# Kernel tuning notes

Measured on AMD Instinct MI355X. Metric: run time of the kernel, lower is better.

The kernel has to match this reference:

```python
import jax, jax.numpy as jnp
import numpy as np

QMAX = 255.0  # 8-bit uniform affine quantization


def _round_ste(x):
    # straight-through estimator round (identity gradient)
    return x + jax.lax.stop_gradient(jnp.round(x) - x)


def _fake_quant(x, scale, zero_point):
    # uniform affine quantize-dequantize, as in DAQuant's UniformAffineQuantizer
    zp = _round_ste(zero_point)
    q = jnp.clip(_round_ste(x / scale) + zp, 0.0, QMAX)
    return (q - zp) * scale


def setup_inputs() -> dict:
    key = jax.random.key(0)
    k1, k2, k3, k4, k5 = jax.random.split(key, 5)
    B, S, H, I = 64, 197, 1024, 4096
    hidden_states = jax.random.normal(k1, (B, S, H), dtype=jnp.float32)
    weight = jax.random.normal(k2, (I, H), dtype=jnp.float32) * 0.02
    bias = jax.random.normal(k3, (I,), dtype=jnp.float32) * 0.02
    # per-output-channel weight quant params, per-tensor activation quant params
    w_scale = jax.random.uniform(k4, (I, 1), dtype=jnp.float32) * 1e-3 + 1e-4
    w_zero = jnp.full((I, 1), 128.0, dtype=jnp.float32)
    a_scale = jnp.float32(8.0 / QMAX)  # covers roughly [-4, 4] of activations
    a_zero = jnp.float32(128.0)
    return {
        "hidden_states": hidden_states,
        "weight": weight,
        "bias": bias,
        "w_scale": w_scale,
        "w_zero": w_zero,
        "a_scale": a_scale,
        "a_zero": a_zero,
    }


def reference(hidden_states, weight, bias, w_scale, w_zero, a_scale, a_zero):
    # fake-quant activation (per-tensor) and weight (per-output-channel)
    x_dq = _fake_quant(hidden_states, a_scale, a_zero)        # [B,S,H]
    w_dq = _fake_quant(weight, w_scale, w_zero)               # [I,H]
    y = jnp.einsum('bsh,ih->bsi', x_dq, w_dq) + bias          # [B,S,I]
    return jax.nn.gelu(y, approximate=False)                  # exact GELU (torch default)
```

## Files before the change

kernel.cpp:

```cpp
#include <hip/hip_runtime.h>
#include <hip/hip_bf16.h>

typedef __attribute__((ext_vector_type(4))) int i32x4;
typedef __attribute__((ext_vector_type(4))) float f32x4;

#define K_DIM 1024
#define I_DIM 4096
#define BK3 64
#define NT3 (K_DIM / BK3)

__device__ __forceinline__ float fakeq_int(float x, float s, float zp) {
    float q = fminf(fmaxf(rintf(x / s) + zp, 0.0f), 255.0f);
    return q - zp;
}

__device__ __forceinline__ float gelu_tanh(float y) {
    float y2 = y * y;
    float z = y * fmaf(0.0356774081f, y2, 0.7978845608f);
    return y / (1.0f + __expf(-2.0f * z));
}

__global__ void quant_x_kernel(const float* __restrict__ x, signed char* __restrict__ Aq,
                               const float* __restrict__ a_scale, const float* __restrict__ a_zero,
                               long long n) {
    long long i = ((long long)blockIdx.x * blockDim.x + threadIdx.x) * 8;
    if (i >= n) return;
    float s = a_scale[0];
    float zp = rintf(a_zero[0]);
    float4 v0 = *(const float4*)(x + i);
    float4 v1 = *(const float4*)(x + i + 4);
    int q0 = (int)fakeq_int(v0.x, s, zp), q1 = (int)fakeq_int(v0.y, s, zp);
    int q2 = (int)fakeq_int(v0.z, s, zp), q3 = (int)fakeq_int(v0.w, s, zp);
    int q4 = (int)fakeq_int(v1.x, s, zp), q5 = (int)fakeq_int(v1.y, s, zp);
    int q6 = (int)fakeq_int(v1.z, s, zp), q7 = (int)fakeq_int(v1.w, s, zp);
    int lo = (q0 & 255) | ((q1 & 255) << 8) | ((q2 & 255) << 16) | ((q3 & 255) << 24);
    int hi = (q4 & 255) | ((q5 & 255) << 8) | ((q6 & 255) << 16) | ((q7 & 255) << 24);
    *(int2*)(Aq + i) = make_int2(lo, hi);
}

__global__ void quant_w_kernel(const float* __restrict__ w, signed char* __restrict__ Wq,
                               const float* __restrict__ w_scale, const float* __restrict__ w_zero,
                               long long n) {
    long long i = ((long long)blockIdx.x * blockDim.x + threadIdx.x) * 8;
    if (i >= n) return;
    long long row = i >> 10;
    float s = w_scale[row];
    float zp = rintf(w_zero[row]);
    float4 v0 = *(const float4*)(w + i);
    float4 v1 = *(const float4*)(w + i + 4);
    int q0 = (int)fakeq_int(v0.x, s, zp), q1 = (int)fakeq_int(v0.y, s, zp);
    int q2 = (int)fakeq_int(v0.z, s, zp), q3 = (int)fakeq_int(v0.w, s, zp);
    int q4 = (int)fakeq_int(v1.x, s, zp), q5 = (int)fakeq_int(v1.y, s, zp);
    int q6 = (int)fakeq_int(v1.z, s, zp), q7 = (int)fakeq_int(v1.w, s, zp);
    int lo = (q0 & 255) | ((q1 & 255) << 8) | ((q2 & 255) << 16) | ((q3 & 255) << 24);
    int hi = (q4 & 255) | ((q5 & 255) << 8) | ((q6 & 255) << 16) | ((q7 & 255) << 24);
    *(int2*)(Wq + i) = make_int2(lo, hi);
}

#define GLL(SRC, DST)                                                         \
    __builtin_amdgcn_global_load_lds(                                         \
        (const __attribute__((address_space(1))) void*)(SRC),                 \
        (__attribute__((address_space(3))) void*)(DST), 16, 0, 0)

#define STAGE(TT, BUF)                                          \
    do {                                                        \
        GLL(pA0 + (TT) * BK3, As + (BUF) * 8192 + dA);          \
        GLL(pA1 + (TT) * BK3, As + (BUF) * 8192 + 4096 + dA);   \
        GLL(pB0 + (TT) * BK3, Bs + (BUF) * 8192 + dA);          \
        GLL(pB1 + (TT) * BK3, Bs + (BUF) * 8192 + 4096 + dA);   \
    } while (0)

__global__ __launch_bounds__(256, 3) void gemm_gelu_kernel(
    const signed char* __restrict__ Aq,
    const signed char* __restrict__ Wq,
    const float* __restrict__ bias,
    const float* __restrict__ w_scale,
    const float* __restrict__ a_scale,
    float* __restrict__ out,
    int M, int Ntiles) {
    __shared__ alignas(16) signed char As[3 * 128 * BK3];
    __shared__ alignas(16) signed char Bs[3 * 128 * BK3];

    int nwg = gridDim.x, bid = blockIdx.x;
    int xcd = bid & 7, lin = bid >> 3;
    int q8 = nwg >> 3, r8 = nwg & 7;
    int swz = (xcd < r8 ? xcd * (q8 + 1) : r8 * (q8 + 1) + (xcd - r8) * q8) + lin;
    int mt = swz / Ntiles, nt = swz % Ntiles;

    int tid = threadIdx.x;
    int wave = tid >> 6, lane = tid & 63;
    int wr = wave >> 1, wc = wave & 1;

    long long mrow0 = (long long)mt * 128;
    int ncol0 = nt * 128;

    int r0 = tid >> 2;
    int slotsrc = ((tid & 3) - ((tid >> 3) & 3)) & 3;
    long long mmax = (long long)M - 1;
    long long raA0 = mrow0 + r0;        if (raA0 > mmax) raA0 = mmax;
    long long raA1 = mrow0 + 64 + r0;   if (raA1 > mmax) raA1 = mmax;
    const signed char* pA0 = Aq + raA0 * K_DIM + slotsrc * 16;
    const signed char* pA1 = Aq + raA1 * K_DIM + slotsrc * 16;
    const signed char* pB0 = Wq + ((long long)ncol0 + r0) * K_DIM + slotsrc * 16;
    const signed char* pB1 = Wq + ((long long)ncol0 + 64 + r0) * K_DIM + slotsrc * 16;
    int dA = tid * 16;

    int koffb = (((lane >> 4) + ((lane >> 1) & 3)) & 3) * 16;
    int arowb = wr * 64 + (lane & 15);
    int browb = wc * 64 + (lane & 15);

    i32x4 acc[4][4];
#pragma unroll
    for (int m = 0; m < 4; ++m)
#pragma unroll
        for (int n = 0; n < 4; ++n) acc[m][n] = (i32x4)0;

    STAGE(0, 0);
    STAGE(1, 1);
    asm volatile("s_waitcnt vmcnt(4)" ::: "memory");
    __builtin_amdgcn_s_barrier();

    int buf = 0, bs2 = 2;
    for (int t = 0; t < NT3; ++t) {
        if (t + 2 < NT3) STAGE(t + 2, bs2);

        i32x4 a[4], b[4];
#pragma unroll
        for (int mi = 0; mi < 4; ++mi)
            a[mi] = *(const i32x4*)(As + buf * 8192 + (arowb + mi * 16) * BK3 + koffb);
#pragma unroll
        for (int n = 0; n < 4; ++n)
            b[n] = *(const i32x4*)(Bs + buf * 8192 + (browb + n * 16) * BK3 + koffb);

        __builtin_amdgcn_s_setprio(1);
#pragma unroll
        for (int mi = 0; mi < 4; ++mi)
#pragma unroll
            for (int n = 0; n < 4; ++n)
                acc[mi][n] = __builtin_amdgcn_mfma_i32_16x16x64_i8(a[mi], b[n], acc[mi][n], 0, 0, 0);
        __builtin_amdgcn_s_setprio(0);

        if (t + 2 < NT3) {
            asm volatile("s_waitcnt vmcnt(4)" ::: "memory");
        } else if (t + 1 < NT3) {
            asm volatile("s_waitcnt vmcnt(0)" ::: "memory");
        }
        if (t + 1 < NT3) __builtin_amdgcn_s_barrier();

        buf = (buf == 2) ? 0 : buf + 1;
        bs2 = (bs2 == 2) ? 0 : bs2 + 1;
    }

    float asc = a_scale[0];
    long long row0 = mrow0 + wr * 64;
    int colb = ncol0 + wc * 64 + (lane & 15);
    int rsubE = (lane >> 4) * 4;
    bool fullTile = (mrow0 + 128 <= (long long)M);
    if (fullTile) {
#pragma unroll
        for (int n = 0; n < 4; ++n) {
            int col = colb + n * 16;
            float sc = asc * w_scale[col];
            float bz = bias[col];
#pragma unroll
            for (int m = 0; m < 4; ++m) {
                long long rb = row0 + m * 16 + rsubE;
#pragma unroll
                for (int rg = 0; rg < 4; ++rg) {
                    float y = (float)acc[m][n][rg] * sc + bz;
                    out[(rb + rg) * I_DIM + col] = gelu_tanh(y);
                }
            }
        }
    } else {
#pragma unroll
        for (int n = 0; n < 4; ++n) {
            int col = colb + n * 16;
            float sc = asc * w_scale[col];
            float bz = bias[col];
#pragma unroll
            for (int m = 0; m < 4; ++m) {
                long long rb = row0 + m * 16 + rsubE;
#pragma unroll
                for (int rg = 0; rg < 4; ++rg) {
                    long long rowi = rb + rg;
                    if (rowi < M) {
                        float y = (float)acc[m][n][rg] * sc + bz;
                        out[rowi * I_DIM + col] = gelu_tanh(y);
                    }
                }
            }
        }
    }
}

__global__ void fallback_kernel(const float* __restrict__ x, const float* __restrict__ w,
                                const float* __restrict__ bias, const float* __restrict__ w_scale,
                                const float* __restrict__ w_zero, const float* __restrict__ a_scale,
                                const float* __restrict__ a_zero, float* __restrict__ out,
                                long long M) {
    long long gid = (long long)blockIdx.x * blockDim.x + threadIdx.x;
    if (gid >= M * I_DIM) return;
    int i = (int)(gid & (I_DIM - 1));
    long long row = gid >> 12;
    float as = a_scale[0], az = rintf(a_zero[0]);
    float wsc = w_scale[i], wz = rintf(w_zero[i]);
    const float* xr = x + row * K_DIM;
    const float* wrp = w + (long long)i * K_DIM;
    float accf = 0.0f;
    for (int k = 0; k < K_DIM; ++k)
        accf += fakeq_int(xr[k], as, az) * fakeq_int(wrp[k], wsc, wz);
    float y = accf * as * wsc + bias[i];
    out[gid] = 0.5f * y * (1.0f + erff(y * 0.70710678118654752f));
}

extern "C" void kernel_launch(void* const* d_in, const int* in_sizes, int n_in,
                              void* d_out, int out_size, void* d_ws, size_t ws_size,
                              hipStream_t stream) {
    const float* x       = (const float*)d_in[0];
    const float* w       = (const float*)d_in[1];
    const float* bias    = (const float*)d_in[2];
    const float* w_scale = (const float*)d_in[3];
    const float* w_zero  = (const float*)d_in[4];
    const float* a_scale = (const float*)d_in[5];
    const float* a_zero  = (const float*)d_in[6];
    float* out = (float*)d_out;

    long long n_x = in_sizes[0];
    long long M = n_x / K_DIM;
    size_t needA = ((size_t)n_x + 255) & ~(size_t)255;
    size_t needW = (size_t)I_DIM * K_DIM;

    if (ws_size >= needA + needW) {
        signed char* Aq = (signed char*)d_ws;
        signed char* Wq = (signed char*)((char*)d_ws + needA);

        long long blocksX = (n_x / 8 + 255) / 256;
        quant_x_kernel<<<(int)blocksX, 256, 0, stream>>>(x, Aq, a_scale, a_zero, n_x);

        long long ndw = (long long)I_DIM * K_DIM;
        long long blocksW = (ndw / 8 + 255) / 256;
        quant_w_kernel<<<(int)blocksW, 256, 0, stream>>>(w, Wq, w_scale, w_zero, ndw);

        int Mtiles = (int)((M + 127) / 128);
        int Ntiles = I_DIM / 128;
        gemm_gelu_kernel<<<Mtiles * Ntiles, 256, 0, stream>>>(Aq, Wq, bias, w_scale, a_scale,
                                                              out, (int)M, Ntiles);
    } else {
        long long total = M * I_DIM;
        long long blocks = (total + 255) / 256;
        fallback_kernel<<<(int)blocks, 256, 0, stream>>>(x, w, bias, w_scale, w_zero,
                                                         a_scale, a_zero, out, M);
    }
}
```

Before: 130.7 us.

## Load weight operand directly into registers, bypassing LDS staging

The weight (B) tiles are no longer staged through shared memory. Each wave now loads its own MFMA B fragments straight from global memory into a double-buffered register array, one k-step ahead. Only the activation tiles still go through LDS, now in a 4-deep ring, and the main loop is fully unrolled with the wait counts adjusted and the priority toggles removed. This cuts LDS traffic and barrier-protected copies. In exchange, B is loaded twice from global/L2 (once per wave row), uses more registers, and gives less latency hiding for the B loads.

```diff
diff --git a/kernel.cpp b/kernel.cpp
--- a/kernel.cpp
+++ b/kernel.cpp
@@ -2,12 +2,11 @@
 #include <hip/hip_bf16.h>
 
 typedef __attribute__((ext_vector_type(4))) int i32x4;
-typedef __attribute__((ext_vector_type(4))) float f32x4;
 
 #define K_DIM 1024
 #define I_DIM 4096
 #define BK3 64
-#define NT3 (K_DIM / BK3)
+#define NT3 16
 
 __device__ __forceinline__ float fakeq_int(float x, float s, float zp) {
     float q = fminf(fmaxf(rintf(x / s) + zp, 0.0f), 255.0f);
@@ -62,12 +61,10 @@
         (const __attribute__((address_space(1))) void*)(SRC),                 \
         (__attribute__((address_space(3))) void*)(DST), 16, 0, 0)
 
-#define STAGE(TT, BUF)                                          \
+#define STAGE_A(TT, BUF)                                        \
     do {                                                        \
         GLL(pA0 + (TT) * BK3, As + (BUF) * 8192 + dA);          \
         GLL(pA1 + (TT) * BK3, As + (BUF) * 8192 + 4096 + dA);   \
-        GLL(pB0 + (TT) * BK3, Bs + (BUF) * 8192 + dA);          \
-        GLL(pB1 + (TT) * BK3, Bs + (BUF) * 8192 + 4096 + dA);   \
     } while (0)
 
 __global__ __launch_bounds__(256, 3) void gemm_gelu_kernel(
@@ -78,8 +75,7 @@
     const float* __restrict__ a_scale,
     float* __restrict__ out,
     int M, int Ntiles) {
-    __shared__ alignas(16) signed char As[3 * 128 * BK3];
-    __shared__ alignas(16) signed char Bs[3 * 128 * BK3];
+    __shared__ alignas(16) signed char As[4 * 128 * BK3];
 
     int nwg = gridDim.x, bid = blockIdx.x;
     int xcd = bid & 7, lin = bid >> 3;
@@ -101,13 +97,16 @@
     long long raA1 = mrow0 + 64 + r0;   if (raA1 > mmax) raA1 = mmax;
     const signed char* pA0 = Aq + raA0 * K_DIM + slotsrc * 16;
     const signed char* pA1 = Aq + raA1 * K_DIM + slotsrc * 16;
-    const signed char* pB0 = Wq + ((long long)ncol0 + r0) * K_DIM + slotsrc * 16;
-    const signed char* pB1 = Wq + ((long long)ncol0 + 64 + r0) * K_DIM + slotsrc * 16;
     int dA = tid * 16;
 
     int koffb = (((lane >> 4) + ((lane >> 1) & 3)) & 3) * 16;
     int arowb = wr * 64 + (lane & 15);
-    int browb = wc * 64 + (lane & 15);
+
+    int colbase = ncol0 + wc * 64;
+    const signed char* pB[4];
+#pragma unroll
+    for (int n = 0; n < 4; ++n)
+        pB[n] = Wq + ((long long)colbase + n * 16 + (lane & 15)) * K_DIM + (lane >> 4) * 16;
 
     i32x4 acc[4][4];
 #pragma unroll
@@ -115,45 +114,46 @@
 #pragma unroll
         for (int n = 0; n < 4; ++n) acc[m][n] = (i32x4)0;
 
-    STAGE(0, 0);
-    STAGE(1, 1);
-    asm volatile("s_waitcnt vmcnt(4)" ::: "memory");
+    i32x4 breg[2][4];
+
+    STAGE_A(0, 0);
+    STAGE_A(1, 1);
+#pragma unroll
+    for (int n = 0; n < 4; ++n) breg[0][n] = *(const i32x4*)(pB[n]);
+    asm volatile("s_waitcnt vmcnt(0)" ::: "memory");
     __builtin_amdgcn_s_barrier();
 
-    int buf = 0, bs2 = 2;
+#pragma unroll
     for (int t = 0; t < NT3; ++t) {
-        if (t + 2 < NT3) STAGE(t + 2, bs2);
-
-        i32x4 a[4], b[4];
+        if (t + 2 < NT3) STAGE_A(t + 2, (t + 2) & 3);
+        if (t + 1 < NT3) {
+#pragma unroll
+            for (int n = 0; n < 4; ++n)
+                breg[(t + 1) & 1][n] = *(const i32x4*)(pB[n] + (t + 1) * BK3);
+        }
+
+        i32x4 a[4];
 #pragma unroll
         for (int mi = 0; mi < 4; ++mi)
-            a[mi] = *(const i32x4*)(As + buf * 8192 + (arowb + mi * 16) * BK3 + koffb);
-#pragma unroll
-        for (int n = 0; n < 4; ++n)
-            b[n] = *(const i32x4*)(Bs + buf * 8192 + (browb + n * 16) * BK3 + koffb);
-
-        __builtin_amdgcn_s_setprio(1);
+            a[mi] = *(const i32x4*)(As + (t & 3) * 8192 + (arowb + mi * 16) * BK3 + koffb);
+
 #pragma unroll
         for (int mi = 0; mi < 4; ++mi)
 #pragma unroll
             for (int n = 0; n < 4; ++n)
-                acc[mi][n] = __builtin_amdgcn_mfma_i32_16x16x64_i8(a[mi], b[n], acc[mi][n], 0, 0, 0);
-        __builtin_amdgcn_s_setprio(0);
+                acc[mi][n] = __builtin_amdgcn_mfma_i32_16x16x64_i8(a[mi], breg[t & 1][n], acc[mi][n], 0, 0, 0);
 
         if (t + 2 < NT3) {
+            asm volatile("s_waitcnt vmcnt(6)" ::: "memory");
+        } else if (t + 1 < NT3) {
             asm volatile("s_waitcnt vmcnt(4)" ::: "memory");
-        } else if (t + 1 < NT3) {
-            asm volatile("s_waitcnt vmcnt(0)" ::: "memory");
         }
         if (t + 1 < NT3) __builtin_amdgcn_s_barrier();
-
-        buf = (buf == 2) ? 0 : buf + 1;
-        bs2 = (bs2 == 2) ? 0 : bs2 + 1;
     }
 
     float asc = a_scale[0];
     long long row0 = mrow0 + wr * 64;
-    int colb = ncol0 + wc * 64 + (lane & 15);
+    int colb = colbase + (lane & 15);
     int rsubE = (lane >> 4) * 4;
     bool fullTile = (mrow0 + 128 <= (long long)M);
     if (fullTile) {
```

New measurement: 164.7 us. 1.26x slower.
